# Kernel optimization log

Measured on AMD Instinct MI355X. Metric: run time of the kernel, lower is better.

The kernel has to match this reference:

```python
import jax, jax.numpy as jnp
import numpy as np

# Graph sizes: 3-hop neighbor-sampled minibatch (PyG NeighborSampler layout)
N0, N1, N2, N3 = 1_000_000, 100_000, 10_000, 1024   # node counts per hop
E0, E1, E2 = 1_500_000, 150_000, 15_360             # edge counts per hop
D, H = 128, 512                                     # in_out_channels, hidden_channels


def setup_inputs() -> dict:
    key = jax.random.key(0)
    ks = jax.random.split(key, 16)

    def lin(k, fi, fo):  # Glorot-ish init for a Linear weight (in, out)
        return jax.random.normal(k, (fi, fo), jnp.float32) / np.sqrt(fi).astype(np.float32)

    return {
        "x": jax.random.normal(ks[0], (N0, D), jnp.float32),
        "ei0_src": jax.random.randint(ks[1], (E0,), 0, N0),
        "ei0_dst": jax.random.randint(ks[2], (E0,), 0, N1),
        "ei1_src": jax.random.randint(ks[3], (E1,), 0, N1),
        "ei1_dst": jax.random.randint(ks[4], (E1,), 0, N2),
        "ei2_src": jax.random.randint(ks[5], (E2,), 0, N2),
        "ei2_dst": jax.random.randint(ks[6], (E2,), 0, N3),
        "W_l0": lin(ks[7], D, H), "b_l0": jnp.zeros((H,), jnp.float32), "W_r0": lin(ks[8], D, H),
        "W_l1": lin(ks[9], H, H), "b_l1": jnp.zeros((H,), jnp.float32), "W_r1": lin(ks[10], H, H),
        "W_l2": lin(ks[11], H, D), "b_l2": jnp.zeros((D,), jnp.float32), "W_r2": lin(ks[12], H, D),
    }


def _sage_conv(x_src, n_tgt, src, dst, W_l, b_l, W_r):
    """PyG SAGEConv (mean aggr): lin_l(scatter_mean(x_src[src] -> dst)) + lin_r(x_tgt)."""
    x_tgt = x_src[:n_tgt]                       # targets are the first n_tgt nodes
    msg = x_src[src]                            # [E, F_in] neighbor gather
    agg_sum = jax.ops.segment_sum(msg, dst, num_segments=n_tgt)
    cnt = jax.ops.segment_sum(jnp.ones((src.shape[0], 1), msg.dtype), dst, num_segments=n_tgt)
    agg_mean = agg_sum / jnp.maximum(cnt, 1.0)
    return agg_mean @ W_l + b_l + x_tgt @ W_r


def reference(x, ei0_src, ei0_dst, ei1_src, ei1_dst, ei2_src, ei2_dst,
              W_l0, b_l0, W_r0, W_l1, b_l1, W_r1, W_l2, b_l2, W_r2):
    h = _sage_conv(x, N1, ei0_src, ei0_dst, W_l0, b_l0, W_r0)
    h = jax.nn.gelu(h, approximate=False)       # F.gelu (exact erf); eval-mode dropout = identity
    h = _sage_conv(h, N2, ei1_src, ei1_dst, W_l1, b_l1, W_r1)
    h = jax.nn.gelu(h, approximate=False)
    h = _sage_conv(h, N3, ei2_src, ei2_dst, W_l2, b_l2, W_r2)
    return h  # [N3, D]
```

## Files before the change

kernel.cpp:

```cpp
#include <hip/hip_runtime.h>
#include <math.h>

static const int N0 = 1000000, N1 = 100000, N2 = 10000, N3 = 1024;
static const int E0 = 1500000, E1 = 150000, E2 = 15360;
static const int D = 128, H = 512;

typedef unsigned short u16;
typedef unsigned int u32;
typedef __attribute__((ext_vector_type(8))) short bf16x8;
typedef __attribute__((ext_vector_type(4))) float f32x4;
typedef __attribute__((ext_vector_type(4))) unsigned short us4;
typedef __attribute__((ext_vector_type(4))) int i32x4;

__device__ __forceinline__ u16 bhi(float v) {
    return (u16)(__float_as_uint(v) >> 16);
}
__device__ __forceinline__ u16 blo(float v) {
    float hf = __uint_as_float(__float_as_uint(v) & 0xFFFF0000u);
    return (u16)(__float_as_uint(v - hf) >> 16);
}

__global__ void count_kernel(const int* __restrict__ dst, int* __restrict__ cnt, int E) {
    int e = blockIdx.x * blockDim.x + threadIdx.x;
    if (e < E) atomicAdd(cnt + dst[e], 1);
}

__global__ __launch_bounds__(1024)
void scan_kernel(const int* __restrict__ cnt, int* __restrict__ offs, int N, int E) {
    __shared__ int part[1024];
    int t = threadIdx.x;
    int per = (N + 1023) >> 10;
    int beg = t * per, end = min(beg + per, N);
    int s = 0;
    for (int i = beg; i < end; ++i) s += cnt[i];
    part[t] = s;
    __syncthreads();
    for (int off = 1; off < 1024; off <<= 1) {
        int v = (t >= off) ? part[t - off] : 0;
        __syncthreads();
        part[t] += v;
        __syncthreads();
    }
    int run = (t == 0) ? 0 : part[t - 1];
    for (int i = beg; i < end; ++i) { offs[i] = run; run += cnt[i]; }
    if (t == 0) offs[N] = E;
}

__global__ void fill_kernel(const int* __restrict__ dst, const int* __restrict__ src,
                            const int* __restrict__ offs, int* __restrict__ cur,
                            int* __restrict__ sorted, int E) {
    int e = blockIdx.x * blockDim.x + threadIdx.x;
    if (e < E) {
        int d = dst[e];
        int p = offs[d] + atomicAdd(cur + d, 1);
        sorted[p] = src[e];
    }
}

__global__ void split_rows_kernel(const float* __restrict__ src, u16* __restrict__ dst,
                                  int total) {
    int i = (blockIdx.x * 256 + threadIdx.x) * 4;
    if (i >= total) return;
    f32x4 v = *(const f32x4*)(src + i);
    us4 hv = { bhi(v.x), bhi(v.y), bhi(v.z), bhi(v.w) };
    us4 lv = { blo(v.x), blo(v.y), blo(v.z), blo(v.w) };
    *(us4*)(dst + i) = hv;
    *(us4*)(dst + (size_t)total + i) = lv;
}

__global__ void wsplit_kernel(const float* __restrict__ W, u16* __restrict__ bt,
                              int K, int N) {
    int idx = blockIdx.x * 256 + threadIdx.x;
    if (idx >= K * N) return;
    int k = idx / N, n = idx - k * N;
    float v = W[idx];
    bt[(size_t)n * K + k] = bhi(v);
    bt[(size_t)N * K + (size_t)n * K + k] = blo(v);
}

__global__ __launch_bounds__(256)
void gather_mean_128p(const float* __restrict__ x, const int* __restrict__ offs,
                      const int* __restrict__ srt, u16* __restrict__ aggP, int Ntgt) {
    int wid = (int)((blockIdx.x * 256 + threadIdx.x) >> 6);
    int lane = threadIdx.x & 63;
    if (wid >= Ntgt) return;
    int beg = offs[wid], end = offs[wid + 1];
    float ax = 0.f, ay = 0.f;
    int e = beg;
    for (; e + 8 <= end; e += 8) {
        int s0 = srt[e], s1 = srt[e + 1], s2 = srt[e + 2], s3 = srt[e + 3];
        int s4 = srt[e + 4], s5 = srt[e + 5], s6 = srt[e + 6], s7 = srt[e + 7];
        float2 v0 = ((const float2*)(x + (size_t)s0 * 128))[lane];
        float2 v1 = ((const float2*)(x + (size_t)s1 * 128))[lane];
        float2 v2 = ((const float2*)(x + (size_t)s2 * 128))[lane];
        float2 v3 = ((const float2*)(x + (size_t)s3 * 128))[lane];
        float2 v4 = ((const float2*)(x + (size_t)s4 * 128))[lane];
        float2 v5 = ((const float2*)(x + (size_t)s5 * 128))[lane];
        float2 v6 = ((const float2*)(x + (size_t)s6 * 128))[lane];
        float2 v7 = ((const float2*)(x + (size_t)s7 * 128))[lane];
        ax += v0.x + v1.x + v2.x + v3.x + v4.x + v5.x + v6.x + v7.x;
        ay += v0.y + v1.y + v2.y + v3.y + v4.y + v5.y + v6.y + v7.y;
    }
    for (; e < end; ++e) {
        int s = srt[e];
        float2 v = ((const float2*)(x + (size_t)s * 128))[lane];
        ax += v.x; ay += v.y;
    }
    float inv = 1.0f / (float)max(end - beg, 1);
    ax *= inv; ay *= inv;
    size_t stride = (size_t)Ntgt * 128;
    u32 hw = (u32)bhi(ax) | ((u32)bhi(ay) << 16);
    u32 lw = (u32)blo(ax) | ((u32)blo(ay) << 16);
    ((u32*)aggP)[(size_t)wid * 64 + lane] = hw;
    ((u32*)(aggP + stride))[(size_t)wid * 64 + lane] = lw;
}

__global__ __launch_bounds__(256)
void gather_mean_512p(const float* __restrict__ x, const int* __restrict__ offs,
                      const int* __restrict__ srt, u16* __restrict__ aggP, int Ntgt) {
    int gw = (int)((blockIdx.x * 256 + threadIdx.x) >> 6);
    int lane = threadIdx.x & 63;
    int node = gw >> 1, half = gw & 1;
    if (node >= Ntgt) return;
    int beg = offs[node], end = offs[node + 1];
    int co = half * 256 + lane * 4;
    float4 acc = make_float4(0.f, 0.f, 0.f, 0.f);
    int e = beg;
    for (; e + 4 <= end; e += 4) {
        int s0 = srt[e], s1 = srt[e + 1], s2 = srt[e + 2], s3 = srt[e + 3];
        float4 v0 = *(const float4*)(x + (size_t)s0 * 512 + co);
        float4 v1 = *(const float4*)(x + (size_t)s1 * 512 + co);
        float4 v2 = *(const float4*)(x + (size_t)s2 * 512 + co);
        float4 v3 = *(const float4*)(x + (size_t)s3 * 512 + co);
        acc.x += v0.x + v1.x + v2.x + v3.x;
        acc.y += v0.y + v1.y + v2.y + v3.y;
        acc.z += v0.z + v1.z + v2.z + v3.z;
        acc.w += v0.w + v1.w + v2.w + v3.w;
    }
    for (; e < end; ++e) {
        int s = srt[e];
        float4 v = *(const float4*)(x + (size_t)s * 512 + co);
        acc.x += v.x; acc.y += v.y; acc.z += v.z; acc.w += v.w;
    }
    float inv = 1.0f / (float)max(end - beg, 1);
    acc.x *= inv; acc.y *= inv; acc.z *= inv; acc.w *= inv;
    size_t stride = (size_t)Ntgt * 512;
    us4 hv = { bhi(acc.x), bhi(acc.y), bhi(acc.z), bhi(acc.w) };
    us4 lv = { blo(acc.x), blo(acc.y), blo(acc.z), blo(acc.w) };
    *(us4*)(aggP + (size_t)node * 512 + co) = hv;
    *(us4*)(aggP + stride + (size_t)node * 512 + co) = lv;
}

#define LDK 40

template <int BM, bool GELU>
__global__ __launch_bounds__(256)
void combine_mfma(const u16* __restrict__ A0P, const u16* __restrict__ A1P,
                  const u16* __restrict__ Bt0, const u16* __restrict__ Bt1,
                  const float* __restrict__ bias, float* __restrict__ out,
                  int M, int K, int N) {
    constexpr int NJ = (BM == 128) ? 4 : 2;
    __shared__ u16 As_hi[BM][LDK];
    __shared__ u16 As_lo[BM][LDK];
    __shared__ u16 Bs_hi[128][LDK];
    __shared__ u16 Bs_lo[128][LDK];

    int t = threadIdx.x;
    int lane = t & 63, wid = t >> 6;
    int wm = (BM == 128) ? (wid >> 1) * 64 : 0;
    int wn = (BM == 128) ? (wid & 1) * 64 : wid * 32;
    int m0 = blockIdx.y * BM, n0 = blockIdx.x * 128;

    int sr = t >> 2;
    int sc = (t & 3) * 8;

    int fr = lane & 15, kg = lane >> 4;

    f32x4 acc[4][NJ] = {};

    size_t strideA = (size_t)M * K;
    size_t strideB = (size_t)N * K;

    for (int p = 0; p < 2; ++p) {
        const u16* Ah = p ? A1P : A0P;
        const u16* Al = Ah + strideA;
        const u16* Bh = p ? Bt1 : Bt0;
        const u16* Bl = Bh + strideB;

        for (int k0 = 0; k0 < K; k0 += 32) {
#pragma unroll
            for (int it = 0; it < BM / 64; ++it) {
                int row = it * 64 + sr;
                int rg = m0 + row;
                i32x4 hv = {0, 0, 0, 0}, lv = {0, 0, 0, 0};
                if (rg < M) {
                    size_t goff = (size_t)rg * K + k0 + sc;
                    hv = *(const i32x4*)(Ah + goff);
                    lv = *(const i32x4*)(Al + goff);
                }
                *(i32x4*)&As_hi[row][sc] = hv;
                *(i32x4*)&As_lo[row][sc] = lv;
            }
#pragma unroll
            for (int it = 0; it < 2; ++it) {
                int nn = it * 64 + sr;
                size_t goff = (size_t)(n0 + nn) * K + k0 + sc;
                *(i32x4*)&Bs_hi[nn][sc] = *(const i32x4*)(Bh + goff);
                *(i32x4*)&Bs_lo[nn][sc] = *(const i32x4*)(Bl + goff);
            }
            __syncthreads();

            bf16x8 a_hi[4], a_lo[4], b_hi[NJ], b_lo[NJ];
#pragma unroll
            for (int i = 0; i < 4; ++i) {
                a_hi[i] = *(const bf16x8*)&As_hi[wm + i * 16 + fr][kg * 8];
                a_lo[i] = *(const bf16x8*)&As_lo[wm + i * 16 + fr][kg * 8];
            }
#pragma unroll
            for (int j = 0; j < NJ; ++j) {
                b_hi[j] = *(const bf16x8*)&Bs_hi[wn + j * 16 + fr][kg * 8];
                b_lo[j] = *(const bf16x8*)&Bs_lo[wn + j * 16 + fr][kg * 8];
            }
#pragma unroll
            for (int i = 0; i < 4; ++i)
#pragma unroll
                for (int j = 0; j < NJ; ++j) {
                    acc[i][j] = __builtin_amdgcn_mfma_f32_16x16x32_bf16(
                        a_hi[i], b_hi[j], acc[i][j], 0, 0, 0);
                    acc[i][j] = __builtin_amdgcn_mfma_f32_16x16x32_bf16(
                        a_hi[i], b_lo[j], acc[i][j], 0, 0, 0);
                    acc[i][j] = __builtin_amdgcn_mfma_f32_16x16x32_bf16(
                        a_lo[i], b_hi[j], acc[i][j], 0, 0, 0);
                }
            __syncthreads();
        }
    }

    int fq = lane >> 4;
#pragma unroll
    for (int i = 0; i < 4; ++i) {
        int rbase = m0 + wm + i * 16 + fq * 4;
#pragma unroll
        for (int j = 0; j < NJ; ++j) {
            int c = n0 + wn + j * 16 + fr;
            float bv = bias[c];
#pragma unroll
            for (int r = 0; r < 4; ++r) {
                int row = rbase + r;
                if (row < M) {
                    float v = acc[i][j][r] + bv;
                    if (GELU) v = 0.5f * v * (1.0f + erff(v * 0.70710678118654752f));
                    out[(size_t)row * N + c] = v;
                }
            }
        }
    }
}

extern "C" void kernel_launch(void* const* d_in, const int* in_sizes, int n_in,
                              void* d_out, int out_size, void* d_ws, size_t ws_size,
                              hipStream_t stream) {
    const float* x       = (const float*)d_in[0];
    const int*   ei0_src = (const int*)d_in[1];
    const int*   ei0_dst = (const int*)d_in[2];
    const int*   ei1_src = (const int*)d_in[3];
    const int*   ei1_dst = (const int*)d_in[4];
    const int*   ei2_src = (const int*)d_in[5];
    const int*   ei2_dst = (const int*)d_in[6];
    const float* W_l0    = (const float*)d_in[7];
    const float* b_l0    = (const float*)d_in[8];
    const float* W_r0    = (const float*)d_in[9];
    const float* W_l1    = (const float*)d_in[10];
    const float* b_l1    = (const float*)d_in[11];
    const float* W_r1    = (const float*)d_in[12];
    const float* W_l2    = (const float*)d_in[13];
    const float* b_l2    = (const float*)d_in[14];
    const float* W_r2    = (const float*)d_in[15];
    float* out = (float*)d_out;
    char*  ws  = (char*)d_ws;

    size_t off = 0;
    auto alloc = [&](size_t bytes) { char* p = ws + off; off += (bytes + 255) & ~(size_t)255; return p; };

    float* h1    = (float*)alloc((size_t)N1 * H * 4);
    float* h2    = (float*)alloc((size_t)N2 * H * 4);
    u16*   aggP0 = (u16*)alloc((size_t)N1 * D * 2 * 2);
    u16*   xP0   = (u16*)alloc((size_t)N1 * D * 2 * 2);
    u16*   aggP1 = (u16*)alloc((size_t)N2 * H * 2 * 2);
    u16*   h1P   = (u16*)alloc((size_t)N2 * H * 2 * 2);
    u16*   aggP2 = (u16*)alloc((size_t)N3 * H * 2 * 2);
    u16*   h2P   = (u16*)alloc((size_t)N3 * H * 2 * 2);
    u16*   bt0l  = (u16*)alloc((size_t)H * D * 2 * 2);
    u16*   bt0r  = (u16*)alloc((size_t)H * D * 2 * 2);
    u16*   bt1l  = (u16*)alloc((size_t)H * H * 2 * 2);
    u16*   bt1r  = (u16*)alloc((size_t)H * H * 2 * 2);
    u16*   bt2l  = (u16*)alloc((size_t)D * H * 2 * 2);
    u16*   bt2r  = (u16*)alloc((size_t)D * H * 2 * 2);
    int*   offs0 = (int*)alloc((size_t)(N1 + 1) * 4);
    int*   cnt0  = (int*)alloc((size_t)2 * N1 * 4);
    int*   srt0  = (int*)alloc((size_t)E0 * 4);
    int*   offs1 = (int*)alloc((size_t)(N2 + 1) * 4);
    int*   cnt1  = (int*)alloc((size_t)2 * N2 * 4);
    int*   srt1  = (int*)alloc((size_t)E1 * 4);
    int*   offs2 = (int*)alloc((size_t)(N3 + 1) * 4);
    int*   cnt2  = (int*)alloc((size_t)2 * N3 * 4);
    int*   srt2  = (int*)alloc((size_t)E2 * 4);
    int* cur0 = cnt0 + N1;
    int* cur1 = cnt1 + N2;
    int* cur2 = cnt2 + N3;

    hipMemsetAsync(cnt0, 0, 2 * N1 * sizeof(int), stream);
    hipMemsetAsync(cnt1, 0, 2 * N2 * sizeof(int), stream);
    hipMemsetAsync(cnt2, 0, 2 * N3 * sizeof(int), stream);
    count_kernel<<<(E0 + 255) / 256, 256, 0, stream>>>(ei0_dst, cnt0, E0);
    count_kernel<<<(E1 + 255) / 256, 256, 0, stream>>>(ei1_dst, cnt1, E1);
    count_kernel<<<(E2 + 255) / 256, 256, 0, stream>>>(ei2_dst, cnt2, E2);
    scan_kernel<<<1, 1024, 0, stream>>>(cnt0, offs0, N1, E0);
    scan_kernel<<<1, 1024, 0, stream>>>(cnt1, offs1, N2, E1);
    scan_kernel<<<1, 1024, 0, stream>>>(cnt2, offs2, N3, E2);
    fill_kernel<<<(E0 + 255) / 256, 256, 0, stream>>>(ei0_dst, ei0_src, offs0, cur0, srt0, E0);
    fill_kernel<<<(E1 + 255) / 256, 256, 0, stream>>>(ei1_dst, ei1_src, offs1, cur1, srt1, E1);
    fill_kernel<<<(E2 + 255) / 256, 256, 0, stream>>>(ei2_dst, ei2_src, offs2, cur2, srt2, E2);

    wsplit_kernel<<<(D * H + 255) / 256, 256, 0, stream>>>(W_l0, bt0l, D, H);
    wsplit_kernel<<<(D * H + 255) / 256, 256, 0, stream>>>(W_r0, bt0r, D, H);
    wsplit_kernel<<<(H * H + 255) / 256, 256, 0, stream>>>(W_l1, bt1l, H, H);
    wsplit_kernel<<<(H * H + 255) / 256, 256, 0, stream>>>(W_r1, bt1r, H, H);
    wsplit_kernel<<<(H * D + 255) / 256, 256, 0, stream>>>(W_l2, bt2l, H, D);
    wsplit_kernel<<<(H * D + 255) / 256, 256, 0, stream>>>(W_r2, bt2r, H, D);
    split_rows_kernel<<<(N1 * D / 4 + 255) / 256, 256, 0, stream>>>(x, xP0, N1 * D);

    gather_mean_128p<<<(N1 + 3) / 4, 256, 0, stream>>>(x, offs0, srt0, aggP0, N1);
    combine_mfma<128, true><<<dim3(H / 128, (N1 + 127) / 128), 256, 0, stream>>>(
        aggP0, xP0, bt0l, bt0r, b_l0, h1, N1, D, H);

    split_rows_kernel<<<(N2 * H / 4 + 255) / 256, 256, 0, stream>>>(h1, h1P, N2 * H);
    gather_mean_512p<<<(2 * N2 + 3) / 4, 256, 0, stream>>>(h1, offs1, srt1, aggP1, N2);
    combine_mfma<64, true><<<dim3(H / 128, (N2 + 63) / 64), 256, 0, stream>>>(
        aggP1, h1P, bt1l, bt1r, b_l1, h2, N2, H, H);

    split_rows_kernel<<<(N3 * H / 4 + 255) / 256, 256, 0, stream>>>(h2, h2P, N3 * H);
    gather_mean_512p<<<(2 * N3 + 3) / 4, 256, 0, stream>>>(h2, offs2, srt2, aggP2, N3);
    combine_mfma<64, false><<<dim3(D / 128, (N3 + 63) / 64), 256, 0, stream>>>(
        aggP2, h2P, bt2l, bt2r, b_l2, out, N3, H, D);
}
```

Baseline: 1.433 ms.

## Batch CSR build and weight split kernels, fuse hi/lo plane emission into GEMM epilogue

The three count, scan and fill launches are merged into single launches, and the six weight-split launches become one. The combine GEMM now writes the bf16 hi/lo planes for the next layer's target rows directly in its epilogue, which removes the separate split_rows passes over h1 and h2. It also uses a 1D grid remapped so that the four N-tiles sharing an M-tile group run together for better L2 reuse. The 512-wide gather is unrolled to eight neighbors. Costs include extra scattered u16 stores in the GEMM epilogue and wasted early-exit blocks from grid padding.

```diff
diff --git a/kernel.cpp b/kernel.cpp
--- a/kernel.cpp
+++ b/kernel.cpp
@@ -20,14 +20,24 @@
     return (u16)(__float_as_uint(v - hf) >> 16);
 }
 
-__global__ void count_kernel(const int* __restrict__ dst, int* __restrict__ cnt, int E) {
-    int e = blockIdx.x * blockDim.x + threadIdx.x;
-    if (e < E) atomicAdd(cnt + dst[e], 1);
+__global__ void count_all(const int* __restrict__ d0, const int* __restrict__ d1,
+                          const int* __restrict__ d2, int* __restrict__ c0,
+                          int* __restrict__ c1, int* __restrict__ c2) {
+    int e = blockIdx.x * 256 + threadIdx.x;
+    if (e < E0) atomicAdd(c0 + d0[e], 1);
+    if (e < E1) atomicAdd(c1 + d1[e], 1);
+    if (e < E2) atomicAdd(c2 + d2[e], 1);
 }
 
 __global__ __launch_bounds__(1024)
-void scan_kernel(const int* __restrict__ cnt, int* __restrict__ offs, int N, int E) {
+void scan_all(const int* __restrict__ c0, int* __restrict__ o0,
+              const int* __restrict__ c1, int* __restrict__ o1,
+              const int* __restrict__ c2, int* __restrict__ o2) {
     __shared__ int part[1024];
+    const int* cnt; int* offs; int N, E;
+    if (blockIdx.x == 0)      { cnt = c0; offs = o0; N = N1; E = E0; }
+    else if (blockIdx.x == 1) { cnt = c1; offs = o1; N = N2; E = E1; }
+    else                      { cnt = c2; offs = o2; N = N3; E = E2; }
     int t = threadIdx.x;
     int per = (N + 1023) >> 10;
     int beg = t * per, end = min(beg + per, N);
@@ -46,15 +56,44 @@
     if (t == 0) offs[N] = E;
 }
 
-__global__ void fill_kernel(const int* __restrict__ dst, const int* __restrict__ src,
-                            const int* __restrict__ offs, int* __restrict__ cur,
-                            int* __restrict__ sorted, int E) {
-    int e = blockIdx.x * blockDim.x + threadIdx.x;
-    if (e < E) {
-        int d = dst[e];
-        int p = offs[d] + atomicAdd(cur + d, 1);
-        sorted[p] = src[e];
-    }
+__global__ void fill_all(const int* __restrict__ d0, const int* __restrict__ s0,
+                         const int* __restrict__ of0, int* __restrict__ cu0, int* __restrict__ sr0,
+                         const int* __restrict__ d1, const int* __restrict__ s1,
+                         const int* __restrict__ of1, int* __restrict__ cu1, int* __restrict__ sr1,
+                         const int* __restrict__ d2, const int* __restrict__ s2,
+                         const int* __restrict__ of2, int* __restrict__ cu2, int* __restrict__ sr2) {
+    int e = blockIdx.x * 256 + threadIdx.x;
+    if (e < E0) { int d = d0[e]; sr0[of0[d] + atomicAdd(cu0 + d, 1)] = s0[e]; }
+    if (e < E1) { int d = d1[e]; sr1[of1[d] + atomicAdd(cu1 + d, 1)] = s1[e]; }
+    if (e < E2) { int d = d2[e]; sr2[of2[d] + atomicAdd(cu2 + d, 1)] = s2[e]; }
+}
+
+__device__ __forceinline__ void wsplit1(const float* W, u16* bt, int idx, int K, int N) {
+    int k = idx / N, n = idx - k * N;
+    float v = W[idx];
+    bt[(size_t)n * K + k] = bhi(v);
+    bt[(size_t)N * K + (size_t)n * K + k] = blo(v);
+}
+__global__ void wsplit_all(const float* __restrict__ Wl0, u16* __restrict__ b0l,
+                           const float* __restrict__ Wr0, u16* __restrict__ b0r,
+                           const float* __restrict__ Wl1, u16* __restrict__ b1l,
+                           const float* __restrict__ Wr1, u16* __restrict__ b1r,
+                           const float* __restrict__ Wl2, u16* __restrict__ b2l,
+                           const float* __restrict__ Wr2, u16* __restrict__ b2r) {
+    const int S0 = D * H;
+    const int S1 = H * H;
+    int idx = blockIdx.x * 256 + threadIdx.x;
+    if (idx < S0)                 { wsplit1(Wl0, b0l, idx, D, H); return; }
+    idx -= S0;
+    if (idx < S0)                 { wsplit1(Wr0, b0r, idx, D, H); return; }
+    idx -= S0;
+    if (idx < S1)                 { wsplit1(Wl1, b1l, idx, H, H); return; }
+    idx -= S1;
+    if (idx < S1)                 { wsplit1(Wr1, b1r, idx, H, H); return; }
+    idx -= S1;
+    if (idx < S0)                 { wsplit1(Wl2, b2l, idx, H, D); return; }
+    idx -= S0;
+    if (idx < S0)                 { wsplit1(Wr2, b2r, idx, H, D); return; }
 }
 
 __global__ void split_rows_kernel(const float* __restrict__ src, u16* __restrict__ dst,
@@ -66,16 +105,6 @@
     us4 lv = { blo(v.x), blo(v.y), blo(v.z), blo(v.w) };
     *(us4*)(dst + i) = hv;
     *(us4*)(dst + (size_t)total + i) = lv;
-}
-
-__global__ void wsplit_kernel(const float* __restrict__ W, u16* __restrict__ bt,
-                              int K, int N) {
-    int idx = blockIdx.x * 256 + threadIdx.x;
-    if (idx >= K * N) return;
-    int k = idx / N, n = idx - k * N;
-    float v = W[idx];
-    bt[(size_t)n * K + k] = bhi(v);
-    bt[(size_t)N * K + (size_t)n * K + k] = blo(v);
 }
 
 __global__ __launch_bounds__(256)
@@ -126,16 +155,21 @@
     int co = half * 256 + lane * 4;
     float4 acc = make_float4(0.f, 0.f, 0.f, 0.f);
     int e = beg;
-    for (; e + 4 <= end; e += 4) {
+    for (; e + 8 <= end; e += 8) {
         int s0 = srt[e], s1 = srt[e + 1], s2 = srt[e + 2], s3 = srt[e + 3];
+        int s4 = srt[e + 4], s5 = srt[e + 5], s6 = srt[e + 6], s7 = srt[e + 7];
         float4 v0 = *(const float4*)(x + (size_t)s0 * 512 + co);
         float4 v1 = *(const float4*)(x + (size_t)s1 * 512 + co);
         float4 v2 = *(const float4*)(x + (size_t)s2 * 512 + co);
         float4 v3 = *(const float4*)(x + (size_t)s3 * 512 + co);
-        acc.x += v0.x + v1.x + v2.x + v3.x;
-        acc.y += v0.y + v1.y + v2.y + v3.y;
-        acc.z += v0.z + v1.z + v2.z + v3.z;
-        acc.w += v0.w + v1.w + v2.w + v3.w;
+        float4 v4 = *(const float4*)(x + (size_t)s4 * 512 + co);
+        float4 v5 = *(const float4*)(x + (size_t)s5 * 512 + co);
+        float4 v6 = *(const float4*)(x + (size_t)s6 * 512 + co);
+        float4 v7 = *(const float4*)(x + (size_t)s7 * 512 + co);
+        acc.x += v0.x + v1.x + v2.x + v3.x + v4.x + v5.x + v6.x + v7.x;
+        acc.y += v0.y + v1.y + v2.y + v3.y + v4.y + v5.y + v6.y + v7.y;
+        acc.z += v0.z + v1.z + v2.z + v3.z + v4.z + v5.z + v6.z + v7.z;
+        acc.w += v0.w + v1.w + v2.w + v3.w + v4.w + v5.w + v6.w + v7.w;
     }
     for (; e < end; ++e) {
         int s = srt[e];
@@ -153,11 +187,12 @@
 
 #define LDK 40
 
-template <int BM, bool GELU>
+template <int BM, int NX, bool GELU, bool PLANES>
 __global__ __launch_bounds__(256)
 void combine_mfma(const u16* __restrict__ A0P, const u16* __restrict__ A1P,
                   const u16* __restrict__ Bt0, const u16* __restrict__ Bt1,
                   const float* __restrict__ bias, float* __restrict__ out,
+                  u16* __restrict__ outP, int MP,
                   int M, int K, int N) {
     constexpr int NJ = (BM == 128) ? 4 : 2;
     __shared__ u16 As_hi[BM][LDK];
@@ -165,11 +200,17 @@
     __shared__ u16 Bs_hi[128][LDK];
     __shared__ u16 Bs_lo[128][LDK];
 
+    int L = blockIdx.x;
+    int m_t, n_t;
+    if (NX == 4) { n_t = (L >> 3) & 3; m_t = (L & 7) + ((L >> 5) << 3); }
+    else         { n_t = L % NX;       m_t = L / NX; }
+    int m0 = m_t * BM, n0 = n_t * 128;
+    if (m0 >= M) return;
+
     int t = threadIdx.x;
     int lane = t & 63, wid = t >> 6;
     int wm = (BM == 128) ? (wid >> 1) * 64 : 0;
     int wn = (BM == 128) ? (wid & 1) * 64 : wid * 32;
-    int m0 = blockIdx.y * BM, n0 = blockIdx.x * 128;
 
     int sr = t >> 2;
     int sc = (t & 3) * 8;
@@ -251,6 +292,11 @@
                     float v = acc[i][j][r] + bv;
                     if (GELU) v = 0.5f * v * (1.0f + erff(v * 0.70710678118654752f));
                     out[(size_t)row * N + c] = v;
+                    if (PLANES && row < MP) {
+                        size_t po = (size_t)row * N + c;
+                        outP[po] = bhi(v);
+                        outP[(size_t)MP * N + po] = blo(v);
+                    }
                 }
             }
         }
@@ -297,50 +343,48 @@
     u16*   bt2l  = (u16*)alloc((size_t)D * H * 2 * 2);
     u16*   bt2r  = (u16*)alloc((size_t)D * H * 2 * 2);
     int*   offs0 = (int*)alloc((size_t)(N1 + 1) * 4);
-    int*   cnt0  = (int*)alloc((size_t)2 * N1 * 4);
+    int*   offs1 = (int*)alloc((size_t)(N2 + 1) * 4);
+    int*   offs2 = (int*)alloc((size_t)(N3 + 1) * 4);
+    int*   cntAll = (int*)alloc((size_t)2 * (N1 + N2 + N3) * 4);
     int*   srt0  = (int*)alloc((size_t)E0 * 4);
-    int*   offs1 = (int*)alloc((size_t)(N2 + 1) * 4);
-    int*   cnt1  = (int*)alloc((size_t)2 * N2 * 4);
     int*   srt1  = (int*)alloc((size_t)E1 * 4);
-    int*   offs2 = (int*)alloc((size_t)(N3 + 1) * 4);
-    int*   cnt2  = (int*)alloc((size_t)2 * N3 * 4);
     int*   srt2  = (int*)alloc((size_t)E2 * 4);
-    int* cur0 = cnt0 + N1;
-    int* cur1 = cnt1 + N2;
-    int* cur2 = cnt2 + N3;
-
-    hipMemsetAsync(cnt0, 0, 2 * N1 * sizeof(int), stream);
-    hipMemsetAsync(cnt1, 0, 2 * N2 * sizeof(int), stream);
-    hipMemsetAsync(cnt2, 0, 2 * N3 * sizeof(int), stream);
-    count_kernel<<<(E0 + 255) / 256, 256, 0, stream>>>(ei0_dst, cnt0, E0);
-    count_kernel<<<(E1 + 255) / 256, 256, 0, stream>>>(ei1_dst, cnt1, E1);
-    count_kernel<<<(E2 + 255) / 256, 256, 0, stream>>>(ei2_dst, cnt2, E2);
-    scan_kernel<<<1, 1024, 0, stream>>>(cnt0, offs0, N1, E0);
-    scan_kernel<<<1, 1024, 0, stream>>>(cnt1, offs1, N2, E1);
-    scan_kernel<<<1, 1024, 0, stream>>>(cnt2, offs2, N3, E2);
-    fill_kernel<<<(E0 + 255) / 256, 256, 0, stream>>>(ei0_dst, ei0_src, offs0, cur0, srt0, E0);
-    fill_kernel<<<(E1 + 255) / 256, 256, 0, stream>>>(ei1_dst, ei1_src, offs1, cur1, srt1, E1);
-    fill_kernel<<<(E2 + 255) / 256, 256, 0, stream>>>(ei2_dst, ei2_src, offs2, cur2, srt2, E2);
-
-    wsplit_kernel<<<(D * H + 255) / 256, 256, 0, stream>>>(W_l0, bt0l, D, H);
-    wsplit_kernel<<<(D * H + 255) / 256, 256, 0, stream>>>(W_r0, bt0r, D, H);
-    wsplit_kernel<<<(H * H + 255) / 256, 256, 0, stream>>>(W_l1, bt1l, H, H);
-    wsplit_kernel<<<(H * H + 255) / 256, 256, 0, stream>>>(W_r1, bt1r, H, H);
-    wsplit_kernel<<<(H * D + 255) / 256, 256, 0, stream>>>(W_l2, bt2l, H, D);
-    wsplit_kernel<<<(H * D + 255) / 256, 256, 0, stream>>>(W_r2, bt2r, H, D);
+    int* cnt0 = cntAll;          int* cur0 = cnt0 + N1;
+    int* cnt1 = cur0 + N1;       int* cur1 = cnt1 + N2;
+    int* cnt2 = cur1 + N2;       int* cur2 = cnt2 + N3;
+
+    hipMemsetAsync(cntAll, 0, 2 * (N1 + N2 + N3) * sizeof(int), stream);
+    count_all<<<(E0 + 255) / 256, 256, 0, stream>>>(ei0_dst, ei1_dst, ei2_dst, cnt0, cnt1, cnt2);
+    scan_all<<<3, 1024, 0, stream>>>(cnt0, offs0, cnt1, offs1, cnt2, offs2);
+    fill_all<<<(E0 + 255) / 256, 256, 0, stream>>>(
+        ei0_dst, ei0_src, offs0, cur0, srt0,
+        ei1_dst, ei1_src, offs1, cur1, srt1,
+        ei2_dst, ei2_src, offs2, cur2, srt2);
+
+    wsplit_all<<<(2 * D * H + 2 * H * H + 2 * H * D + 255) / 256, 256, 0, stream>>>(
+        W_l0, bt0l, W_r0, bt0r, W_l1, bt1l, W_r1, bt1r, W_l2, bt2l, W_r2, bt2r);
     split_rows_kernel<<<(N1 * D / 4 + 255) / 256, 256, 0, stream>>>(x, xP0, N1 * D);
 
     gather_mean_128p<<<(N1 + 3) / 4, 256, 0, stream>>>(x, offs0, srt0, aggP0, N1);
-    combine_mfma<128, true><<<dim3(H / 128, (N1 + 127) / 128), 256, 0, stream>>>(
-        aggP0, xP0, bt0l, bt0r, b_l0, h1, N1, D, H);
-
-    split_rows_kernel<<<(N2 * H / 4 + 255) / 256, 256, 0, stream>>>(h1, h1P, N2 * H);
+    {
+        int Mt = (N1 + 127) / 128;
+        int MtPad = (Mt + 7) & ~7;
+        combine_mfma<128, 4, true, true><<<4 * MtPad, 256, 0, stream>>>(
+            aggP0, xP0, bt0l, bt0r, b_l0, h1, h1P, N2, N1, D, H);
+    }
+
     gather_mean_512p<<<(2 * N2 + 3) / 4, 256, 0, stream>>>(h1, offs1, srt1, aggP1, N2);
-    combine_mfma<64, true><<<dim3(H / 128, (N2 + 63) / 64), 256, 0, stream>>>(
-        aggP1, h1P, bt1l, bt1r, b_l1, h2, N2, H, H);
-
-    split_rows_kernel<<<(N3 * H / 4 + 255) / 256, 256, 0, stream>>>(h2, h2P, N3 * H);
+    {
+        int Mt = (N2 + 63) / 64;
+        int MtPad = (Mt + 7) & ~7;
+        combine_mfma<64, 4, true, true><<<4 * MtPad, 256, 0, stream>>>(
+            aggP1, h1P, bt1l, bt1r, b_l1, h2, h2P, N3, N2, H, H);
+    }
+
     gather_mean_512p<<<(2 * N3 + 3) / 4, 256, 0, stream>>>(h2, offs2, srt2, aggP2, N3);
-    combine_mfma<64, false><<<dim3(D / 128, (N3 + 63) / 64), 256, 0, stream>>>(
-        aggP2, h2P, bt2l, bt2r, b_l2, out, N3, H, D);
-}
+    {
+        int Mt = (N3 + 63) / 64;
+        combine_mfma<64, 1, false, false><<<1 * Mt, 256, 0, stream>>>(
+            aggP2, h2P, bt2l, bt2r, b_l2, out, (u16*)nullptr, 0, N3, H, D);
+    }
+}
```

Measured after the change: 1.379 ms. -3.8%, faster.
